# Kernel tuning notes

Hardware: AMD Instinct MI355X
Metric: run time of the kernel (lower is better)

The kernel has to match this reference:

```python
import jax, jax.numpy as jnp
import numpy as np

B, S, D_MODEL, N_HEADS, D_K, D_V = 2, 2048, 1024, 16, 64, 64


def setup_inputs() -> dict:
    key = jax.random.key(0)
    ks = jax.random.split(key, 11)
    s_in = 1.0 / np.sqrt(D_MODEL)
    s_out = 1.0 / np.sqrt(N_HEADS * D_V)
    return {
        "Q": jax.random.normal(ks[0], (B, S, D_MODEL), jnp.float32),
        "K": jax.random.normal(ks[1], (B, S, D_MODEL), jnp.float32),
        "V": jax.random.normal(ks[2], (B, S, D_MODEL), jnp.float32),
        # per-head projection weights (stacked over heads), Linear-style: y = x @ W + b
        "Wq": jax.random.uniform(ks[3], (N_HEADS, D_MODEL, D_K), jnp.float32, -s_in, s_in),
        "bq": jax.random.uniform(ks[4], (N_HEADS, D_K), jnp.float32, -s_in, s_in),
        "Wk": jax.random.uniform(ks[5], (N_HEADS, D_MODEL, D_K), jnp.float32, -s_in, s_in),
        "bk": jax.random.uniform(ks[6], (N_HEADS, D_K), jnp.float32, -s_in, s_in),
        "Wv": jax.random.uniform(ks[7], (N_HEADS, D_MODEL, D_V), jnp.float32, -s_in, s_in),
        "bv": jax.random.uniform(ks[8], (N_HEADS, D_V), jnp.float32, -s_in, s_in),
        "Wo": jax.random.uniform(ks[9], (N_HEADS * D_V, D_MODEL), jnp.float32, -s_out, s_out),
        "bo": jax.random.uniform(ks[10], (D_MODEL,), jnp.float32, -s_out, s_out),
    }


def reference(Q, K, V, Wq, bq, Wk, bk, Wv, bv, Wo, bo):
    # Per-head projections, batched over heads: [B,H,S,dk/dv]
    QW = jnp.einsum("bsd,hdk->bhsk", Q, Wq) + bq[None, :, None, :]
    KW = jnp.einsum("bsd,hdk->bhsk", K, Wk) + bk[None, :, None, :]
    VW = jnp.einsum("bsd,hdv->bhsv", V, Wv) + bv[None, :, None, :]
    scores = jnp.einsum("bhsk,bhtk->bhst", QW, KW)  # [B,H,S,S]
    # Faithful to torch source: softmax(scores)/d_k**1/2 == softmax(scores)/(2*d_k)
    attn = jax.nn.softmax(scores, axis=-1) * (1.0 / (2.0 * D_K))
    heads = jnp.einsum("bhst,bhtv->bhsv", attn, VW)  # [B,H,S,dv]
    # concat heads along feature dim -> [B,S,H*dv], then output projection
    concat = heads.transpose(0, 2, 1, 3).reshape(B, S, N_HEADS * D_V)
    return concat @ Wo + bo
```

## Files before the change

kernel.cpp:

```cpp
#include <hip/hip_runtime.h>

#define BB 2
#define SS 2048
#define DM 1024
#define HH 16
#define DK 64
#define LOG2E 1.44269504088896340736f

typedef __attribute__((ext_vector_type(8))) short short8;
typedef __attribute__((ext_vector_type(4))) float f32x4;
typedef __attribute__((ext_vector_type(16))) float f32x16;

#define MFMA16(a, b, c) __builtin_amdgcn_mfma_f32_16x16x32_bf16(a, b, c, 0, 0, 0)
#define MFMA32(a, b, c) __builtin_amdgcn_mfma_f32_32x32x16_bf16(a, b, c, 0, 0, 0)

#if __has_builtin(__builtin_amdgcn_exp2f)
#define EXP2(x) __builtin_amdgcn_exp2f(x)
#else
#define EXP2(x) __expf((x) * 0.6931471805599453f)
#endif

#define WAITV(N) asm volatile("s_waitcnt vmcnt(" #N ")" ::: "memory")
#define BAR() __builtin_amdgcn_s_barrier()

static __device__ __forceinline__ unsigned short f2bf(float f) {
    unsigned u = __builtin_bit_cast(unsigned, f);
    u += 0x7fffu + ((u >> 16) & 1u);
    return (unsigned short)(u >> 16);
}
static __device__ __forceinline__ float bf2f(unsigned short u) {
    return __builtin_bit_cast(float, ((unsigned)u) << 16);
}

static __device__ __forceinline__ void gld16(const void* g, void* l) {
    __builtin_amdgcn_global_load_lds(
        (const __attribute__((address_space(1))) unsigned int*)g,
        (__attribute__((address_space(3))) unsigned int*)l, 16, 0, 0);
}

__global__ __launch_bounds__(256) void cvt3_kernel(
    const float* __restrict__ p0, const float* __restrict__ p1,
    const float* __restrict__ p2, unsigned short* __restrict__ o0,
    unsigned short* __restrict__ o1, unsigned short* __restrict__ o2) {
    const int m = blockIdx.y;
    const float* in = m == 0 ? p0 : (m == 1 ? p1 : p2);
    unsigned short* out = m == 0 ? o0 : (m == 1 ? o1 : o2);
    const int i = (blockIdx.x * 256 + threadIdx.x) * 8;
    float4 a = *(const float4*)(in + i);
    float4 b = *(const float4*)(in + i + 4);
    union { unsigned short u[8]; uint4 v; } x;
    x.u[0] = f2bf(a.x); x.u[1] = f2bf(a.y); x.u[2] = f2bf(a.z); x.u[3] = f2bf(a.w);
    x.u[4] = f2bf(b.x); x.u[5] = f2bf(b.y); x.u[6] = f2bf(b.z); x.u[7] = f2bf(b.w);
    *(uint4*)(out + i) = x.v;
}

__global__ __launch_bounds__(256) void wtrans4_kernel(
    const float* __restrict__ Wq, const float* __restrict__ Wk,
    const float* __restrict__ Wv, const float* __restrict__ Wo,
    unsigned short* __restrict__ Wqt, unsigned short* __restrict__ Wkt,
    unsigned short* __restrict__ Wvt, unsigned short* __restrict__ Wot) {
    __shared__ float t[64][65];
    const int which = blockIdx.y;
    const float* in;
    unsigned short* out;
    int r0, c0, C;
    if (which < 3) {
        in = which == 0 ? Wq : (which == 1 ? Wk : Wv);
        out = which == 0 ? Wqt : (which == 1 ? Wkt : Wvt);
        const int h = blockIdx.x >> 4;
        r0 = (blockIdx.x & 15) * 64; c0 = 0; C = DK;
        in += (size_t)h * DM * DK;
        out += (size_t)h * DK * DM;
    } else {
        in = Wo; out = Wot;
        r0 = (blockIdx.x & 15) * 64; c0 = (blockIdx.x >> 4) * 64; C = DM;
    }
    const int lr = threadIdx.x & 63, gg = threadIdx.x >> 6;
    #pragma unroll
    for (int p = 0; p < 16; ++p) {
        const int r = p * 4 + gg;
        t[r][lr] = in[(size_t)(r0 + r) * C + c0 + lr];
    }
    __syncthreads();
    #pragma unroll
    for (int p = 0; p < 16; ++p) {
        const int c = p * 4 + gg;
        out[(size_t)(c0 + c) * DM + r0 + lr] = f2bf(t[lr][c]);
    }
}

#define GSTAGE(Ap, Btp, k0, pp)                                              \
    do {                                                                     \
        _Pragma("unroll")                                                    \
        for (int i = 0; i < 4; ++i) {                                        \
            const int idx = tid + i * 256;                                   \
            const int row = idx >> 3, c8 = (idx & 7) * 8;                    \
            gld16(&Ap[(size_t)(r0 + row) * DM + (k0) + c8], &As[pp][idx * 8]); \
            gld16(&Btp[(size_t)(n0 + row) * DM + (k0) + c8], &Bs[pp][idx * 8]); \
        }                                                                    \
    } while (0)

#define GCOMPUTE(pp)                                                         \
    do {                                                                     \
        _Pragma("unroll")                                                    \
        for (int kc = 0; kc < 2; ++kc) {                                     \
            short8 a[4], b[4];                                               \
            _Pragma("unroll")                                                \
            for (int i = 0; i < 4; ++i) {                                    \
                a[i] = *(const short8*)&As[pp][(wr + i * 16 + lr) * 64 + kc * 32 + lg * 8]; \
                b[i] = *(const short8*)&Bs[pp][(wc + i * 16 + lr) * 64 + kc * 32 + lg * 8]; \
            }                                                                \
            __builtin_amdgcn_s_setprio(1);                                   \
            _Pragma("unroll")                                                \
            for (int mi = 0; mi < 4; ++mi)                                   \
                _Pragma("unroll")                                            \
                for (int ni = 0; ni < 4; ++ni)                               \
                    acc[mi][ni] = MFMA16(a[mi], b[ni], acc[mi][ni]);         \
            __builtin_amdgcn_s_setprio(0);                                   \
        }                                                                    \
    } while (0)

#define GEMM_MAIN(Ap, Btp)                                                   \
    GSTAGE(Ap, Btp, 0, 0);                                                   \
    for (int k = 0; k < 14 * 64; k += 128) {                                 \
        GSTAGE(Ap, Btp, k + 64, 1);                                          \
        WAITV(8); BAR();                                                     \
        GCOMPUTE(0);                                                         \
        BAR();                                                               \
        GSTAGE(Ap, Btp, k + 128, 0);                                         \
        WAITV(8); BAR();                                                     \
        GCOMPUTE(1);                                                         \
        BAR();                                                               \
    }                                                                        \
    GSTAGE(Ap, Btp, 15 * 64, 1);                                             \
    WAITV(8); BAR();                                                         \
    GCOMPUTE(0);                                                             \
    BAR();                                                                   \
    WAITV(0); BAR();                                                         \
    GCOMPUTE(1);

__global__ __launch_bounds__(256) void qkv_gemm_kernel(
    const unsigned short* __restrict__ Qb, const unsigned short* __restrict__ Kb,
    const unsigned short* __restrict__ Vb,
    const unsigned short* __restrict__ Wqt, const unsigned short* __restrict__ Wkt,
    const unsigned short* __restrict__ Wvt,
    const float* __restrict__ bq, const float* __restrict__ bk,
    const float* __restrict__ bv,
    unsigned short* __restrict__ QWp, unsigned short* __restrict__ KWp,
    unsigned short* __restrict__ VWt) {
    __shared__ unsigned short As[2][128 * 64];
    __shared__ unsigned short Bs[2][128 * 64];
    const int z = blockIdx.z;
    const unsigned short* A  = z == 0 ? Qb : (z == 1 ? Kb : Vb);
    const unsigned short* Bt = z == 0 ? Wqt : (z == 1 ? Wkt : Wvt);
    const float* bias = z == 0 ? bq : (z == 1 ? bk : bv);
    const int tid = threadIdx.x;
    const int r0 = blockIdx.x * 128, n0 = blockIdx.y * 128;
    const int w = tid >> 6, lane = tid & 63, lr = lane & 15, lg = lane >> 4;
    const int wr = (w >> 1) * 64, wc = (w & 1) * 64;

    const f32x4 zf = {0.f, 0.f, 0.f, 0.f};
    f32x4 acc[4][4];
    #pragma unroll
    for (int mi = 0; mi < 4; ++mi)
        #pragma unroll
        for (int ni = 0; ni < 4; ++ni) acc[mi][ni] = zf;

    GEMM_MAIN(A, Bt);

    const float scale = (z == 0) ? LOG2E : 1.0f;
    #pragma unroll
    for (int ni = 0; ni < 4; ++ni) {
        const int col = n0 + wc + ni * 16 + lr;
        const float bb = bias[col];
        #pragma unroll
        for (int mi = 0; mi < 4; ++mi) {
            const int rbase = r0 + wr + mi * 16 + lg * 4;
            const f32x4 v = acc[mi][ni];
            if (z == 2) {
                const int b = rbase >> 11, s = rbase & (SS - 1);
                const int h = col >> 6, vv = col & 63;
                union { unsigned short u[4]; unsigned long long q; } x;
                #pragma unroll
                for (int j = 0; j < 4; ++j) x.u[j] = f2bf(v[j] + bb);
                *(unsigned long long*)&VWt[((size_t)(b * HH + h) * 64 + vv) * SS + s] = x.q;
            } else {
                unsigned short* C = z == 0 ? QWp : KWp;
                #pragma unroll
                for (int j = 0; j < 4; ++j)
                    C[(size_t)(rbase + j) * DM + col] = f2bf((v[j] + bb) * scale);
            }
        }
    }
}

__global__ __launch_bounds__(256) void outproj_kernel(
    const unsigned short* __restrict__ A, const unsigned short* __restrict__ Bt,
    const float* __restrict__ bias, float* __restrict__ Cout) {
    __shared__ unsigned short As[2][128 * 64];
    __shared__ unsigned short Bs[2][128 * 64];
    const int tid = threadIdx.x;
    const int r0 = blockIdx.x * 128, n0 = blockIdx.y * 128;
    const int w = tid >> 6, lane = tid & 63, lr = lane & 15, lg = lane >> 4;
    const int wr = (w >> 1) * 64, wc = (w & 1) * 64;

    const f32x4 zf = {0.f, 0.f, 0.f, 0.f};
    f32x4 acc[4][4];
    #pragma unroll
    for (int mi = 0; mi < 4; ++mi)
        #pragma unroll
        for (int ni = 0; ni < 4; ++ni) acc[mi][ni] = zf;

    GEMM_MAIN(A, Bt);

    #pragma unroll
    for (int ni = 0; ni < 4; ++ni) {
        const int col = n0 + wc + ni * 16 + lr;
        const float bb = bias[col];
        #pragma unroll
        for (int mi = 0; mi < 4; ++mi) {
            const int rbase = r0 + wr + mi * 16 + lg * 4;
            const f32x4 v = acc[mi][ni];
            #pragma unroll
            for (int j = 0; j < 4; ++j)
                Cout[(size_t)(rbase + j) * DM + col] = v[j] + bb;
        }
    }
}

#define FRAG(buf, row, col) \
    (*(const short8*)&buf[(row) * 64 + ((col) ^ (((row) & 7) << 3))])

__global__ __launch_bounds__(256, 2) void attn_kernel(
    const unsigned short* __restrict__ QW,
    const unsigned short* __restrict__ KW,
    const unsigned short* __restrict__ VWt,
    unsigned short* __restrict__ CC) {
    __shared__ unsigned short Ks[2][64 * 64];
    __shared__ unsigned short Vs[2][64 * 64];
    const int tid = threadIdx.x;
    const int w = tid >> 6, lane = tid & 63;
    const int ql = lane & 31, hi = lane >> 5, hi8 = hi * 8;

    const int wgid = blockIdx.x;
    const int kk = wgid >> 3;
    const int bh = (kk >> 4) * 8 + (wgid & 7);
    const int b = bh >> 4, h = bh & 15;
    const int row0 = (kk & 15) * 128;
    const int q = row0 + w * 32 + ql;

    short8 qf[4];
    const unsigned short* Qp = QW + ((size_t)b * SS + q) * DM + h * DK;
    #pragma unroll
    for (int kc = 0; kc < 4; ++kc)
        qf[kc] = *(const short8*)(Qp + kc * 16 + hi8);

    const unsigned short* Kp = KW + (size_t)b * SS * DM + h * DK;
    const unsigned short* Vt = VWt + (size_t)bh * 64 * SS;

    const int sidx0 = tid, sidx1 = tid + 256;
    const int srow0 = sidx0 >> 3, sc0 = ((sidx0 & 7) ^ (srow0 & 7)) * 8;
    const int srow1 = sidx1 >> 3, sc1 = ((sidx1 & 7) ^ (srow1 & 7)) * 8;

#define STAGE(t0, pp)                                                        \
    do {                                                                     \
        gld16(&Kp[(size_t)((t0) + srow0) * DM + sc0], &Ks[pp][sidx0 * 8]);   \
        gld16(&Vt[(size_t)srow0 * SS + (t0) + sc0], &Vs[pp][sidx0 * 8]);     \
        gld16(&Kp[(size_t)((t0) + srow1) * DM + sc1], &Ks[pp][sidx1 * 8]);   \
        gld16(&Vt[(size_t)srow1 * SS + (t0) + sc1], &Vs[pp][sidx1 * 8]);     \
    } while (0)

    const f32x16 z16 = {0.f};
    const short8 ones = {(short)0x3F80, (short)0x3F80, (short)0x3F80, (short)0x3F80,
                         (short)0x3F80, (short)0x3F80, (short)0x3F80, (short)0x3F80};
    f32x16 o0 = z16, o1 = z16, lv = z16;

#define PACK2(sx, pa0, pa1)                                                      \
    do {                                                                         \
        unsigned x, x2, y, y2, u, u2, v, v2;                                     \
        asm("v_cvt_pk_bf16_f32 %0, %1, %2" : "=v"(x)  : "v"(sx[0]), "v"(sx[1])); \
        asm("v_cvt_pk_bf16_f32 %0, %1, %2" : "=v"(x2) : "v"(sx[2]), "v"(sx[3])); \
        asm("v_cvt_pk_bf16_f32 %0, %1, %2" : "=v"(y)  : "v"(sx[4]), "v"(sx[5])); \
        asm("v_cvt_pk_bf16_f32 %0, %1, %2" : "=v"(y2) : "v"(sx[6]), "v"(sx[7])); \
        asm("v_cvt_pk_bf16_f32 %0, %1, %2" : "=v"(u)  : "v"(sx[8]), "v"(sx[9])); \
        asm("v_cvt_pk_bf16_f32 %0, %1, %2" : "=v"(u2) : "v"(sx[10]), "v"(sx[11])); \
        asm("v_cvt_pk_bf16_f32 %0, %1, %2" : "=v"(v)  : "v"(sx[12]), "v"(sx[13])); \
        asm("v_cvt_pk_bf16_f32 %0, %1, %2" : "=v"(v2) : "v"(sx[14]), "v"(sx[15])); \
        asm("v_permlane32_swap_b32 %0, %1" : "+v"(x),  "+v"(y));                 \
        asm("v_permlane32_swap_b32 %0, %1" : "+v"(x2), "+v"(y2));                \
        asm("v_permlane32_swap_b32 %0, %1" : "+v"(u),  "+v"(v));                 \
        asm("v_permlane32_swap_b32 %0, %1" : "+v"(u2), "+v"(v2));                \
        union { unsigned uu[4]; short8 s8; } k0, k1;                             \
        k0.uu[0] = x; k0.uu[1] = x2; k0.uu[2] = y; k0.uu[3] = y2;                \
        k1.uu[0] = u; k1.uu[1] = u2; k1.uu[2] = v; k1.uu[3] = v2;                \
        pa0 = k0.s8; pa1 = k1.s8;                                                \
    } while (0)

#define COMPUTE(pp)                                                              \
    do {                                                                         \
        f32x16 s0, s1;                                                           \
        __builtin_amdgcn_s_setprio(1);                                           \
        s0 = MFMA32(FRAG(Ks[pp], ql, hi8), qf[0], z16);                          \
        s1 = MFMA32(FRAG(Ks[pp], 32 + ql, hi8), qf[0], z16);                     \
        _Pragma("unroll")                                                        \
        for (int kc = 1; kc < 4; ++kc) {                                         \
            s0 = MFMA32(FRAG(Ks[pp], ql, kc * 16 + hi8), qf[kc], s0);            \
            s1 = MFMA32(FRAG(Ks[pp], 32 + ql, kc * 16 + hi8), qf[kc], s1);       \
        }                                                                        \
        __builtin_amdgcn_s_setprio(0);                                           \
        _Pragma("unroll")                                                        \
        for (int r = 0; r < 16; ++r) s0[r] = EXP2(s0[r]);                        \
        short8 pa0, pa1, pa2, pa3;                                               \
        PACK2(s0, pa0, pa1);                                                     \
        __builtin_amdgcn_s_setprio(1);                                           \
        o0 = MFMA32(FRAG(Vs[pp], ql, hi8), pa0, o0);                             \
        lv = MFMA32(ones, pa0, lv);                                              \
        o1 = MFMA32(FRAG(Vs[pp], 32 + ql, hi8), pa0, o1);                        \
        o0 = MFMA32(FRAG(Vs[pp], ql, 16 + hi8), pa1, o0);                        \
        lv = MFMA32(ones, pa1, lv);                                              \
        o1 = MFMA32(FRAG(Vs[pp], 32 + ql, 16 + hi8), pa1, o1);                   \
        __builtin_amdgcn_s_setprio(0);                                           \
        _Pragma("unroll")                                                        \
        for (int r = 0; r < 16; ++r) s1[r] = EXP2(s1[r]);                        \
        PACK2(s1, pa2, pa3);                                                     \
        __builtin_amdgcn_s_setprio(1);                                           \
        o0 = MFMA32(FRAG(Vs[pp], ql, 32 + hi8), pa2, o0);                        \
        lv = MFMA32(ones, pa2, lv);                                              \
        o1 = MFMA32(FRAG(Vs[pp], 32 + ql, 32 + hi8), pa2, o1);                   \
        o0 = MFMA32(FRAG(Vs[pp], ql, 48 + hi8), pa3, o0);                        \
        lv = MFMA32(ones, pa3, lv);                                              \
        o1 = MFMA32(FRAG(Vs[pp], 32 + ql, 48 + hi8), pa3, o1);                   \
        __builtin_amdgcn_s_setprio(0);                                           \
    } while (0)

    STAGE(0, 0);
    for (int i = 0; i < 30; i += 2) {
        STAGE((i + 1) * 64, 1);
        WAITV(4); BAR();
        COMPUTE(0);
        BAR();
        STAGE((i + 2) * 64, 0);
        WAITV(4); BAR();
        COMPUTE(1);
        BAR();
    }
    STAGE(31 * 64, 1);
    WAITV(4); BAR();
    COMPUTE(0);
    BAR();
    WAITV(0); BAR();
    COMPUTE(1);
#undef STAGE
#undef COMPUTE

    const float inv = 1.0f / (lv[0] * 128.0f);
    unsigned short* cp = CC + ((size_t)b * SS + q) * DM + h * DK;
    #pragma unroll
    for (int vt = 0; vt < 2; ++vt) {
        const f32x16 ov = vt ? o1 : o0;
        #pragma unroll
        for (int m2 = 0; m2 < 4; ++m2) {
            union { unsigned short u[4]; unsigned long long q8; } pk;
            #pragma unroll
            for (int c = 0; c < 4; ++c) pk.u[c] = f2bf(ov[m2 * 4 + c] * inv);
            *(unsigned long long*)(cp + vt * 32 + m2 * 8 + hi * 4) = pk.q8;
        }
    }
}

extern "C" void kernel_launch(void* const* d_in, const int* in_sizes, int n_in,
                              void* d_out, int out_size, void* d_ws, size_t ws_size,
                              hipStream_t stream) {
    const float* Q  = (const float*)d_in[0];
    const float* K  = (const float*)d_in[1];
    const float* V  = (const float*)d_in[2];
    const float* Wq = (const float*)d_in[3];
    const float* bq = (const float*)d_in[4];
    const float* Wk = (const float*)d_in[5];
    const float* bk = (const float*)d_in[6];
    const float* Wv = (const float*)d_in[7];
    const float* bv = (const float*)d_in[8];
    const float* Wo = (const float*)d_in[9];
    const float* bo = (const float*)d_in[10];
    float* out = (float*)d_out;

    unsigned short* ws = (unsigned short*)d_ws;
    const size_t MK = (size_t)BB * SS * DM;
    const size_t WK = (size_t)DM * DM;
    unsigned short* Qb  = ws;
    unsigned short* Kb  = Qb + MK;
    unsigned short* Vb  = Kb + MK;
    unsigned short* Wqt = Vb + MK;
    unsigned short* Wkt = Wqt + WK;
    unsigned short* Wvt = Wkt + WK;
    unsigned short* Wot = Wvt + WK;
    unsigned short* QWp = Wot + WK;
    unsigned short* KWp = QWp + MK;
    unsigned short* VWt = KWp + MK;
    unsigned short* CCp = Qb;

    dim3 blk(256);
    const int M = BB * SS;

    hipLaunchKernelGGL(cvt3_kernel, dim3(MK / 2048, 3), blk, 0, stream,
                       Q, K, V, Qb, Kb, Vb);

    hipLaunchKernelGGL(wtrans4_kernel, dim3(256, 4), blk, 0, stream,
                       Wq, Wk, Wv, Wo, Wqt, Wkt, Wvt, Wot);

    hipLaunchKernelGGL(qkv_gemm_kernel, dim3(M / 128, 8, 3), blk, 0, stream,
                       Qb, Kb, Vb, Wqt, Wkt, Wvt, bq, bk, bv, QWp, KWp, VWt);

    hipLaunchKernelGGL(attn_kernel, dim3(512), blk, 0, stream,
                       QWp, KWp, VWt, CCp);

    hipLaunchKernelGGL(outproj_kernel, dim3(M / 128, 8), blk, 0, stream,
                       CCp, Wot, bo, out);
}
```

Before: 127.1 us.

## Software-pipeline QK^T of next tile with softmax-PV of current tile, triple buffering

Restructures the attention loop so each step computes QK^T scores for tile t+1 while doing exp/pack and PV MFMAs for tile t, using three LDS buffers for K/V and two sets of score registers. This is meant to let MFMA work overlap the exp and bf16 packing latency and to cut the barriers per tile from two pairs to one. It raises LDS use to 48KB per block and increases register pressure, which may hurt the 2-blocks-per-CU occupancy.

```diff
diff --git a/kernel.cpp b/kernel.cpp
--- a/kernel.cpp
+++ b/kernel.cpp
@@ -236,8 +236,8 @@
     const unsigned short* __restrict__ KW,
     const unsigned short* __restrict__ VWt,
     unsigned short* __restrict__ CC) {
-    __shared__ unsigned short Ks[2][64 * 64];
-    __shared__ unsigned short Vs[2][64 * 64];
+    __shared__ unsigned short Ks[3][64 * 64];
+    __shared__ unsigned short Vs[3][64 * 64];
     const int tid = threadIdx.x;
     const int w = tid >> 6, lane = tid & 63;
     const int ql = lane & 31, hi = lane >> 5, hi8 = hi * 8;
@@ -274,6 +274,20 @@
     const short8 ones = {(short)0x3F80, (short)0x3F80, (short)0x3F80, (short)0x3F80,
                          (short)0x3F80, (short)0x3F80, (short)0x3F80, (short)0x3F80};
     f32x16 o0 = z16, o1 = z16, lv = z16;
+    f32x16 sA0, sA1, sB0, sB1;
+
+#define QKT(bQ, sd0, sd1)                                                        \
+    do {                                                                         \
+        __builtin_amdgcn_s_setprio(1);                                           \
+        sd0 = MFMA32(FRAG(Ks[bQ], ql, hi8), qf[0], z16);                         \
+        sd1 = MFMA32(FRAG(Ks[bQ], 32 + ql, hi8), qf[0], z16);                    \
+        _Pragma("unroll")                                                        \
+        for (int kc = 1; kc < 4; ++kc) {                                         \
+            sd0 = MFMA32(FRAG(Ks[bQ], ql, kc * 16 + hi8), qf[kc], sd0);          \
+            sd1 = MFMA32(FRAG(Ks[bQ], 32 + ql, kc * 16 + hi8), qf[kc], sd1);     \
+        }                                                                        \
+        __builtin_amdgcn_s_setprio(0);                                           \
+    } while (0)
 
 #define PACK2(sx, pa0, pa1)                                                      \
     do {                                                                         \
@@ -296,62 +310,62 @@
         pa0 = k0.s8; pa1 = k1.s8;                                                \
     } while (0)
 
-#define COMPUTE(pp)                                                              \
+#define PVT(bP, sx0, sx1)                                                        \
     do {                                                                         \
-        f32x16 s0, s1;                                                           \
+        _Pragma("unroll")                                                        \
+        for (int r = 0; r < 16; ++r) sx0[r] = EXP2(sx0[r]);                      \
+        short8 pa0, pa1, pa2, pa3;                                               \
+        PACK2(sx0, pa0, pa1);                                                    \
         __builtin_amdgcn_s_setprio(1);                                           \
-        s0 = MFMA32(FRAG(Ks[pp], ql, hi8), qf[0], z16);                          \
-        s1 = MFMA32(FRAG(Ks[pp], 32 + ql, hi8), qf[0], z16);                     \
-        _Pragma("unroll")                                                        \
-        for (int kc = 1; kc < 4; ++kc) {                                         \
-            s0 = MFMA32(FRAG(Ks[pp], ql, kc * 16 + hi8), qf[kc], s0);            \
-            s1 = MFMA32(FRAG(Ks[pp], 32 + ql, kc * 16 + hi8), qf[kc], s1);       \
-        }                                                                        \
+        o0 = MFMA32(FRAG(Vs[bP], ql, hi8), pa0, o0);                             \
+        lv = MFMA32(ones, pa0, lv);                                              \
+        o1 = MFMA32(FRAG(Vs[bP], 32 + ql, hi8), pa0, o1);                        \
+        o0 = MFMA32(FRAG(Vs[bP], ql, 16 + hi8), pa1, o0);                        \
+        lv = MFMA32(ones, pa1, lv);                                              \
+        o1 = MFMA32(FRAG(Vs[bP], 32 + ql, 16 + hi8), pa1, o1);                   \
         __builtin_amdgcn_s_setprio(0);                                           \
         _Pragma("unroll")                                                        \
-        for (int r = 0; r < 16; ++r) s0[r] = EXP2(s0[r]);                        \
-        short8 pa0, pa1, pa2, pa3;                                               \
-        PACK2(s0, pa0, pa1);                                                     \
+        for (int r = 0; r < 16; ++r) sx1[r] = EXP2(sx1[r]);                      \
+        PACK2(sx1, pa2, pa3);                                                    \
         __builtin_amdgcn_s_setprio(1);                                           \
-        o0 = MFMA32(FRAG(Vs[pp], ql, hi8), pa0, o0);                             \
-        lv = MFMA32(ones, pa0, lv);                                              \
-        o1 = MFMA32(FRAG(Vs[pp], 32 + ql, hi8), pa0, o1);                        \
-        o0 = MFMA32(FRAG(Vs[pp], ql, 16 + hi8), pa1, o0);                        \
-        lv = MFMA32(ones, pa1, lv);                                              \
-        o1 = MFMA32(FRAG(Vs[pp], 32 + ql, 16 + hi8), pa1, o1);                   \
+        o0 = MFMA32(FRAG(Vs[bP], ql, 32 + hi8), pa2, o0);                        \
+        lv = MFMA32(ones, pa2, lv);                                              \
+        o1 = MFMA32(FRAG(Vs[bP], 32 + ql, 32 + hi8), pa2, o1);                   \
+        o0 = MFMA32(FRAG(Vs[bP], ql, 48 + hi8), pa3, o0);                        \
+        lv = MFMA32(ones, pa3, lv);                                              \
+        o1 = MFMA32(FRAG(Vs[bP], 32 + ql, 48 + hi8), pa3, o1);                   \
         __builtin_amdgcn_s_setprio(0);                                           \
-        _Pragma("unroll")                                                        \
-        for (int r = 0; r < 16; ++r) s1[r] = EXP2(s1[r]);                        \
-        PACK2(s1, pa2, pa3);                                                     \
-        __builtin_amdgcn_s_setprio(1);                                           \
-        o0 = MFMA32(FRAG(Vs[pp], ql, 32 + hi8), pa2, o0);                        \
-        lv = MFMA32(ones, pa2, lv);                                              \
-        o1 = MFMA32(FRAG(Vs[pp], 32 + ql, 32 + hi8), pa2, o1);                   \
-        o0 = MFMA32(FRAG(Vs[pp], ql, 48 + hi8), pa3, o0);                        \
-        lv = MFMA32(ones, pa3, lv);                                              \
-        o1 = MFMA32(FRAG(Vs[pp], 32 + ql, 48 + hi8), pa3, o1);                   \
-        __builtin_amdgcn_s_setprio(0);                                           \
+    } while (0)
+
+#define SUBT(t, bS, bQ, bP, si0, si1, so0, so1)                              \
+    do {                                                                     \
+        STAGE(((t) + 2) * 64, bS);                                           \
+        WAITV(4); BAR();                                                     \
+        QKT(bQ, so0, so1);                                                   \
+        PVT(bP, si0, si1);                                                   \
+        BAR();                                                               \
     } while (0)
 
     STAGE(0, 0);
-    for (int i = 0; i < 30; i += 2) {
-        STAGE((i + 1) * 64, 1);
-        WAITV(4); BAR();
-        COMPUTE(0);
-        BAR();
-        STAGE((i + 2) * 64, 0);
-        WAITV(4); BAR();
-        COMPUTE(1);
-        BAR();
-    }
-    STAGE(31 * 64, 1);
-    WAITV(4); BAR();
-    COMPUTE(0);
-    BAR();
     WAITV(0); BAR();
-    COMPUTE(1);
+    QKT(0, sA0, sA1);
+    STAGE(64, 1);
+
+    for (int tt = 0; tt < 30; tt += 6) {
+        SUBT(tt + 0, 2, 1, 0, sA0, sA1, sB0, sB1);
+        SUBT(tt + 1, 0, 2, 1, sB0, sB1, sA0, sA1);
+        SUBT(tt + 2, 1, 0, 2, sA0, sA1, sB0, sB1);
+        SUBT(tt + 3, 2, 1, 0, sB0, sB1, sA0, sA1);
+        SUBT(tt + 4, 0, 2, 1, sA0, sA1, sB0, sB1);
+        SUBT(tt + 5, 1, 0, 2, sB0, sB1, sA0, sA1);
+    }
+
+    WAITV(0); BAR();
+    QKT(1, sB0, sB1);
+    PVT(0, sA0, sA1);
+    PVT(1, sB0, sB1);
 #undef STAGE
-#undef COMPUTE
+#undef SUBT
 
     const float inv = 1.0f / (lv[0] * 128.0f);
     unsigned short* cp = CC + ((size_t)b * SS + q) * DM + h * DK;
```

Measured after the change: 127.2 us. About the same (+0.1%).

## Double attention KV tile to 128 keys and swizzle GEMM LDS tiles

Applied to the files above, without the earlier changes.

The attention kernel now stages 128 keys per pipeline step instead of 64. This halves the number of barrier and wait rounds and gives four independent QK score MFMA chains per step, with a 16-way XOR swizzle on the wider V tile. Separately, the projection GEMM's LDS tiles get an XOR swizzle on load and read, meant to cut LDS bank conflicts. The cost is twice the LDS for the attention kernel (64KB per block) and more live score registers, which may hurt the two-blocks-per-CU occupancy.

```diff
diff --git a/kernel.cpp b/kernel.cpp
--- a/kernel.cpp
+++ b/kernel.cpp
@@ -23,13 +23,15 @@
 #define WAITV(N) asm volatile("s_waitcnt vmcnt(" #N ")" ::: "memory")
 #define BAR() __builtin_amdgcn_s_barrier()
 
+#define FRAG(buf, row, col) \
+    (*(const short8*)&buf[(row) * 64 + ((col) ^ (((row) & 7) << 3))])
+#define FRAGV(buf, row, col) \
+    (*(const short8*)&buf[(row) * 128 + (((((col) >> 3) ^ ((row) & 15))) << 3)])
+
 static __device__ __forceinline__ unsigned short f2bf(float f) {
     unsigned u = __builtin_bit_cast(unsigned, f);
     u += 0x7fffu + ((u >> 16) & 1u);
     return (unsigned short)(u >> 16);
-}
-static __device__ __forceinline__ float bf2f(unsigned short u) {
-    return __builtin_bit_cast(float, ((unsigned)u) << 16);
 }
 
 static __device__ __forceinline__ void gld16(const void* g, void* l) {
@@ -94,9 +96,10 @@
         _Pragma("unroll")                                                    \
         for (int i = 0; i < 4; ++i) {                                        \
             const int idx = tid + i * 256;                                   \
-            const int row = idx >> 3, c8 = (idx & 7) * 8;                    \
-            gld16(&Ap[(size_t)(r0 + row) * DM + (k0) + c8], &As[pp][idx * 8]); \
-            gld16(&Btp[(size_t)(n0 + row) * DM + (k0) + c8], &Bs[pp][idx * 8]); \
+            const int row = idx >> 3;                                        \
+            const int cs = ((idx & 7) ^ (row & 7)) * 8;                      \
+            gld16(&Ap[(size_t)(r0 + row) * DM + (k0) + cs], &As[pp][idx * 8]); \
+            gld16(&Btp[(size_t)(n0 + row) * DM + (k0) + cs], &Bs[pp][idx * 8]); \
         }                                                                    \
     } while (0)
 
@@ -107,8 +110,8 @@
             short8 a[4], b[4];                                               \
             _Pragma("unroll")                                                \
             for (int i = 0; i < 4; ++i) {                                    \
-                a[i] = *(const short8*)&As[pp][(wr + i * 16 + lr) * 64 + kc * 32 + lg * 8]; \
-                b[i] = *(const short8*)&Bs[pp][(wc + i * 16 + lr) * 64 + kc * 32 + lg * 8]; \
+                a[i] = FRAG(As[pp], wr + i * 16 + lr, kc * 32 + lg * 8);     \
+                b[i] = FRAG(Bs[pp], wc + i * 16 + lr, kc * 32 + lg * 8);     \
             }                                                                \
             __builtin_amdgcn_s_setprio(1);                                   \
             _Pragma("unroll")                                                \
@@ -228,16 +231,13 @@
     }
 }
 
-#define FRAG(buf, row, col) \
-    (*(const short8*)&buf[(row) * 64 + ((col) ^ (((row) & 7) << 3))])
-
 __global__ __launch_bounds__(256, 2) void attn_kernel(
     const unsigned short* __restrict__ QW,
     const unsigned short* __restrict__ KW,
     const unsigned short* __restrict__ VWt,
     unsigned short* __restrict__ CC) {
-    __shared__ unsigned short Ks[2][64 * 64];
-    __shared__ unsigned short Vs[2][64 * 64];
+    __shared__ unsigned short Ks[2][128 * 64];
+    __shared__ unsigned short Vs[2][64 * 128];
     const int tid = threadIdx.x;
     const int w = tid >> 6, lane = tid & 63;
     const int ql = lane & 31, hi = lane >> 5, hi8 = hi * 8;
@@ -258,16 +258,18 @@
     const unsigned short* Kp = KW + (size_t)b * SS * DM + h * DK;
     const unsigned short* Vt = VWt + (size_t)bh * 64 * SS;
 
-    const int sidx0 = tid, sidx1 = tid + 256;
-    const int srow0 = sidx0 >> 3, sc0 = ((sidx0 & 7) ^ (srow0 & 7)) * 8;
-    const int srow1 = sidx1 >> 3, sc1 = ((sidx1 & 7) ^ (srow1 & 7)) * 8;
-
 #define STAGE(t0, pp)                                                        \
     do {                                                                     \
-        gld16(&Kp[(size_t)((t0) + srow0) * DM + sc0], &Ks[pp][sidx0 * 8]);   \
-        gld16(&Vt[(size_t)srow0 * SS + (t0) + sc0], &Vs[pp][sidx0 * 8]);     \
-        gld16(&Kp[(size_t)((t0) + srow1) * DM + sc1], &Ks[pp][sidx1 * 8]);   \
-        gld16(&Vt[(size_t)srow1 * SS + (t0) + sc1], &Vs[pp][sidx1 * 8]);     \
+        _Pragma("unroll")                                                    \
+        for (int i = 0; i < 4; ++i) {                                        \
+            const int idx = tid + i * 256;                                   \
+            const int kr = idx >> 3;                                         \
+            const int kc8 = ((idx & 7) ^ (kr & 7)) * 8;                      \
+            gld16(&Kp[(size_t)((t0) + kr) * DM + kc8], &Ks[pp][idx * 8]);    \
+            const int vr = idx >> 4;                                         \
+            const int vc8 = ((idx & 15) ^ (vr & 15)) * 8;                    \
+            gld16(&Vt[(size_t)vr * SS + (t0) + vc8], &Vs[pp][idx * 8]);      \
+        }                                                                    \
     } while (0)
 
     const f32x16 z16 = {0.f};
@@ -296,62 +298,64 @@
         pa0 = k0.s8; pa1 = k1.s8;                                                \
     } while (0)
 
+#define PVC(pp, sx, c)                                                           \
+    do {                                                                         \
+        _Pragma("unroll")                                                        \
+        for (int r = 0; r < 16; ++r) sx[r] = EXP2(sx[r]);                        \
+        short8 pa0, pa1;                                                         \
+        PACK2(sx, pa0, pa1);                                                     \
+        __builtin_amdgcn_s_setprio(1);                                           \
+        o0 = MFMA32(FRAGV(Vs[pp], ql, (c) * 32 + hi8), pa0, o0);                 \
+        lv = MFMA32(ones, pa0, lv);                                              \
+        o1 = MFMA32(FRAGV(Vs[pp], 32 + ql, (c) * 32 + hi8), pa0, o1);            \
+        o0 = MFMA32(FRAGV(Vs[pp], ql, (c) * 32 + 16 + hi8), pa1, o0);            \
+        lv = MFMA32(ones, pa1, lv);                                              \
+        o1 = MFMA32(FRAGV(Vs[pp], 32 + ql, (c) * 32 + 16 + hi8), pa1, o1);       \
+        __builtin_amdgcn_s_setprio(0);                                           \
+    } while (0)
+
 #define COMPUTE(pp)                                                              \
     do {                                                                         \
-        f32x16 s0, s1;                                                           \
+        f32x16 s0, s1, s2, s3;                                                   \
         __builtin_amdgcn_s_setprio(1);                                           \
         s0 = MFMA32(FRAG(Ks[pp], ql, hi8), qf[0], z16);                          \
         s1 = MFMA32(FRAG(Ks[pp], 32 + ql, hi8), qf[0], z16);                     \
+        s2 = MFMA32(FRAG(Ks[pp], 64 + ql, hi8), qf[0], z16);                     \
+        s3 = MFMA32(FRAG(Ks[pp], 96 + ql, hi8), qf[0], z16);                     \
         _Pragma("unroll")                                                        \
         for (int kc = 1; kc < 4; ++kc) {                                         \
             s0 = MFMA32(FRAG(Ks[pp], ql, kc * 16 + hi8), qf[kc], s0);            \
             s1 = MFMA32(FRAG(Ks[pp], 32 + ql, kc * 16 + hi8), qf[kc], s1);       \
+            s2 = MFMA32(FRAG(Ks[pp], 64 + ql, kc * 16 + hi8), qf[kc], s2);       \
+            s3 = MFMA32(FRAG(Ks[pp], 96 + ql, kc * 16 + hi8), qf[kc], s3);       \
         }                                                                        \
         __builtin_amdgcn_s_setprio(0);                                           \
-        _Pragma("unroll")                                                        \
-        for (int r = 0; r < 16; ++r) s0[r] = EXP2(s0[r]);                        \
-        short8 pa0, pa1, pa2, pa3;                                               \
-        PACK2(s0, pa0, pa1);                                                     \
-        __builtin_amdgcn_s_setprio(1);                                           \
-        o0 = MFMA32(FRAG(Vs[pp], ql, hi8), pa0, o0);                             \
-        lv = MFMA32(ones, pa0, lv);                                              \
-        o1 = MFMA32(FRAG(Vs[pp], 32 + ql, hi8), pa0, o1);                        \
-        o0 = MFMA32(FRAG(Vs[pp], ql, 16 + hi8), pa1, o0);                        \
-        lv = MFMA32(ones, pa1, lv);                                              \
-        o1 = MFMA32(FRAG(Vs[pp], 32 + ql, 16 + hi8), pa1, o1);                   \
-        __builtin_amdgcn_s_setprio(0);                                           \
-        _Pragma("unroll")                                                        \
-        for (int r = 0; r < 16; ++r) s1[r] = EXP2(s1[r]);                        \
-        PACK2(s1, pa2, pa3);                                                     \
-        __builtin_amdgcn_s_setprio(1);                                           \
-        o0 = MFMA32(FRAG(Vs[pp], ql, 32 + hi8), pa2, o0);                        \
-        lv = MFMA32(ones, pa2, lv);                                              \
-        o1 = MFMA32(FRAG(Vs[pp], 32 + ql, 32 + hi8), pa2, o1);                   \
-        o0 = MFMA32(FRAG(Vs[pp], ql, 48 + hi8), pa3, o0);                        \
-        lv = MFMA32(ones, pa3, lv);                                              \
-        o1 = MFMA32(FRAG(Vs[pp], 32 + ql, 48 + hi8), pa3, o1);                   \
-        __builtin_amdgcn_s_setprio(0);                                           \
+        PVC(pp, s0, 0);                                                          \
+        PVC(pp, s1, 1);                                                          \
+        PVC(pp, s2, 2);                                                          \
+        PVC(pp, s3, 3);                                                          \
     } while (0)
 
     STAGE(0, 0);
-    for (int i = 0; i < 30; i += 2) {
-        STAGE((i + 1) * 64, 1);
-        WAITV(4); BAR();
+    for (int t = 0; t < 14; t += 2) {
+        STAGE((t + 1) * 128, 1);
+        WAITV(8); BAR();
         COMPUTE(0);
         BAR();
-        STAGE((i + 2) * 64, 0);
-        WAITV(4); BAR();
+        STAGE((t + 2) * 128, 0);
+        WAITV(8); BAR();
         COMPUTE(1);
         BAR();
     }
-    STAGE(31 * 64, 1);
-    WAITV(4); BAR();
+    STAGE(15 * 128, 1);
+    WAITV(8); BAR();
     COMPUTE(0);
     BAR();
     WAITV(0); BAR();
     COMPUTE(1);
 #undef STAGE
 #undef COMPUTE
+#undef PVC
 
     const float inv = 1.0f / (lv[0] * 128.0f);
     unsigned short* cp = CC + ((size_t)b * SS + q) * DM + h * DK;
```

After: 119.5 us. -6.0%, faster.
